# Performance work log

Hardware: AMD Instinct MI355X
Metric: run time of the kernel (lower is better)

Reference implementation:

```python
import jax, jax.numpy as jnp
import numpy as np

D = 1024
H = 16
HD = D // H  # 64
FF = 4 * D
EPS = 1e-5


def _xavier(key, shape):
    fan_in, fan_out = shape[1], shape[0]
    limit = float(np.sqrt(6.0 / (fan_in + fan_out)))
    return jax.random.uniform(key, shape, jnp.float32, -limit, limit)


def setup_inputs() -> dict:
    key = jax.random.key(0)
    ks = jax.random.split(key, 8)
    x = jax.random.normal(ks[0], (2, 2048, D), jnp.float32)
    return {
        "x": x,
        "w_qkv": _xavier(ks[1], (3 * D, D)),
        "b_qkv": jnp.zeros((3 * D,), jnp.float32),
        "w_out": _xavier(ks[2], (D, D)),
        "b_out": jnp.zeros((D,), jnp.float32),
        "w1": _xavier(ks[3], (FF, D)),
        "b1": jnp.zeros((FF,), jnp.float32),
        "w2": _xavier(ks[4], (D, FF)),
        "b2": jnp.zeros((D,), jnp.float32),
        "ln1_g": jnp.ones((D,), jnp.float32),
        "ln1_b": jnp.zeros((D,), jnp.float32),
        "ln2_g": jnp.ones((D,), jnp.float32),
        "ln2_b": jnp.zeros((D,), jnp.float32),
    }


def _layernorm(x, g, b):
    mu = jnp.mean(x, -1, keepdims=True)
    var = jnp.mean(jnp.square(x - mu), -1, keepdims=True)
    return (x - mu) * jax.lax.rsqrt(var + EPS) * g + b


def reference(x, w_qkv, b_qkv, w_out, b_out, w1, b1, w2, b2,
              ln1_g, ln1_b, ln2_g, ln2_b):
    B, S, _ = x.shape
    # pre-LN attention branch
    h = _layernorm(x, ln1_g, ln1_b)
    qkv = h @ w_qkv.T + b_qkv                      # [B,S,3D]
    qkv = qkv.reshape(B, S, H, 3 * HD).transpose(0, 2, 1, 3)  # [B,H,S,3hd]
    q, k, v = jnp.split(qkv, 3, axis=-1)
    scores = jnp.einsum('bhqd,bhkd->bhqk', q, k) / np.sqrt(HD)
    attn = jax.nn.softmax(scores, axis=-1)
    ctx = jnp.einsum('bhqk,bhkd->bhqd', attn, v)   # [B,H,S,hd]
    ctx = ctx.transpose(0, 2, 1, 3).reshape(B, S, D)
    x = x + (ctx @ w_out.T + b_out)
    # pre-LN MLP branch
    h = _layernorm(x, ln2_g, ln2_b)
    h = jax.nn.relu(h @ w1.T + b1)
    x = x + (h @ w2.T + b2)
    return x
```

## Files before the change

### kernel.cpp

```cpp
#include <hip/hip_runtime.h>
#include <hip/hip_bf16.h>

typedef __attribute__((ext_vector_type(8))) short bf16x8;
typedef __attribute__((ext_vector_type(4))) float f32x4;
typedef __attribute__((ext_vector_type(16))) float f32x16;
typedef __attribute__((ext_vector_type(4))) unsigned short u16x4;
typedef __attribute__((ext_vector_type(4))) unsigned int u32x4;
typedef unsigned short u16;

__device__ __forceinline__ u16 f2bf(float f) {
  unsigned u = __builtin_bit_cast(unsigned, f);
  u += 0x7fffu + ((u >> 16) & 1u);
  return (u16)(u >> 16);
}
__device__ __forceinline__ float bf2f(u16 u) {
  unsigned v = ((unsigned)u) << 16;
  return __builtin_bit_cast(float, v);
}
__device__ __forceinline__ unsigned cvt_pk_bf16(float lo, float hi) {
  unsigned r;
  asm("v_cvt_pk_bf16_f32 %0, %1, %2" : "=v"(r) : "v"(lo), "v"(hi));
  return r;
}
__device__ __forceinline__ float exp2_fast(float x) {
  float r;
  asm("v_exp_f32 %0, %1" : "=v"(r) : "v"(x));
  return r;
}

__device__ __forceinline__ void gl_lds16(const void* g, void* l) {
  __builtin_amdgcn_global_load_lds((const __attribute__((address_space(1))) void*)g,
                                   (__attribute__((address_space(3))) void*)l,
                                   16, 0, 0);
}

__device__ __forceinline__ void bar() {
  asm volatile("" ::: "memory");
  __builtin_amdgcn_s_barrier();
  asm volatile("" ::: "memory");
}

__global__ __launch_bounds__(256) void cvt_all(const float* __restrict__ a,
                                               const float* __restrict__ b,
                                               const float* __restrict__ c,
                                               const float* __restrict__ d,
                                               u16* __restrict__ oa,
                                               u16* __restrict__ ob,
                                               u16* __restrict__ oc,
                                               u16* __restrict__ od) {
  int i = blockIdx.x * 256 + threadIdx.x;
  const int stride = gridDim.x * 256;
  for (; i < 3145728; i += stride) {
    const float* src;
    u16* dst;
    int j;
    if (i < 786432) { src = a; dst = oa; j = i; }
    else if (i < 1048576) { src = b; dst = ob; j = i - 786432; }
    else if (i < 2097152) { src = c; dst = oc; j = i - 1048576; }
    else { src = d; dst = od; j = i - 2097152; }
    float4 v = ((const float4*)src)[j];
    u16x4 o;
    o.x = f2bf(v.x); o.y = f2bf(v.y); o.z = f2bf(v.z); o.w = f2bf(v.w);
    ((u16x4*)dst)[j] = o;
  }
}

__global__ __launch_bounds__(256) void ln_k(const float* __restrict__ x,
                                            const float* __restrict__ g,
                                            const float* __restrict__ b,
                                            u16* __restrict__ out) {
  const int row = blockIdx.x;
  const int t = threadIdx.x;
  const int lane = t & 63, w = t >> 6;
  const float4 v = ((const float4*)(x + (size_t)row * 1024))[t];
  float s = v.x + v.y + v.z + v.w;
  float q = v.x * v.x + v.y * v.y + v.z * v.z + v.w * v.w;
#pragma unroll
  for (int off = 32; off; off >>= 1) {
    s += __shfl_down(s, off);
    q += __shfl_down(q, off);
  }
  __shared__ float red[8];
  if (lane == 0) { red[w] = s; red[4 + w] = q; }
  __syncthreads();
  s = red[0] + red[1] + red[2] + red[3];
  q = red[4] + red[5] + red[6] + red[7];
  const float mu = s * (1.f / 1024.f);
  const float var = q * (1.f / 1024.f) - mu * mu;
  const float rs = rsqrtf(var + 1e-5f);
  const float4 gv = ((const float4*)g)[t];
  const float4 bv = ((const float4*)b)[t];
  u16x4 o;
  o.x = f2bf((v.x - mu) * rs * gv.x + bv.x);
  o.y = f2bf((v.y - mu) * rs * gv.y + bv.y);
  o.z = f2bf((v.z - mu) * rs * gv.z + bv.z);
  o.w = f2bf((v.w - mu) * rs * gv.w + bv.w);
  ((u16x4*)(out + (size_t)row * 1024))[t] = o;
}

template <int BM, int BN, int BK, int TH, int WN, int MR, int NR, int EPI>
__global__ __launch_bounds__(TH, 2) void gemm_rot(const u16* __restrict__ A,
                                                  const u16* __restrict__ B,
                                                  const float* __restrict__ bias,
                                                  const float* __restrict__ res,
                                                  void* __restrict__ outp,
                                                  const int N, const int K) {
  constexpr int GPR = BK / 8;
  constexpr int KS = BK / 32;
  constexpr int AELEMS = BM * BK;
  constexpr int BELEMS = BN * BK;
  constexpr int NC = (BM + BN) * GPR / TH;
  static_assert((BM * GPR) % TH == 0 && ((BM + BN) * GPR) % TH == 0, "");
  __shared__ u16 lds[3][AELEMS + BELEMS];
  const int t = threadIdx.x;
  const int lane = t & 63, w = t >> 6;
  const int wm = w / WN, wn = w % WN;
  const int l15 = lane & 15, lhi = lane >> 4;
  const int nbx = gridDim.x;
  const int nwg = nbx * gridDim.y;
  const int orig = blockIdx.y * nbx + blockIdx.x;
  const int cpx = nwg >> 3;
  const int lid = (orig & 7) * cpx + (orig >> 3);
  const long bm = (long)(lid / nbx) * BM, bn = (long)(lid % nbx) * BN;
  const u16* Ab = A + bm * K;
  const u16* Bb = B + bn * K;
  const int nk = K / BK;

#define STAGE(kt_, bufi)                                                      \
  do {                                                                        \
    const long kk_ = (long)(kt_) * BK;                                        \
    _Pragma("unroll")                                                         \
    for (int j = 0; j < NC; ++j) {                                            \
      const int sj = j * TH + t;                                              \
      const u16* src_;                                                        \
      if ((j + 1) * TH <= BM * GPR) {                                         \
        const int row_ = sj / GPR, grp_ = sj % GPR;                           \
        const int g_ = (BK == 32) ? (grp_ ^ ((row_ >> 1) & 3))                \
                                  : (grp_ ^ (row_ & 7));                      \
        src_ = Ab + (size_t)row_ * K + kk_ + g_ * 8;                          \
      } else {                                                                \
        const int sb_ = sj - BM * GPR;                                        \
        const int row_ = sb_ / GPR, grp_ = sb_ % GPR;                         \
        const int g_ = (BK == 32) ? (grp_ ^ ((row_ >> 1) & 3))                \
                                  : (grp_ ^ (row_ & 7));                      \
        src_ = Bb + (size_t)row_ * K + kk_ + g_ * 8;                          \
      }                                                                       \
      gl_lds16(src_, &lds[bufi][(size_t)(j * TH + w * 64) * 8]);              \
    }                                                                         \
  } while (0)

  f32x4 acc[MR][NR] = {};
  STAGE(0, 0);
  STAGE(1, 1);
  STAGE(2, 2);
  for (int i = 0; i < nk; ++i) {
    if (i + 2 < nk) {
      if constexpr (NC == 3)      asm volatile("s_waitcnt vmcnt(6)" ::: "memory");
      else if constexpr (NC == 4) asm volatile("s_waitcnt vmcnt(8)" ::: "memory");
      else                        asm volatile("s_waitcnt vmcnt(12)" ::: "memory");
    } else if (i + 1 < nk) {
      if constexpr (NC == 3)      asm volatile("s_waitcnt vmcnt(3)" ::: "memory");
      else if constexpr (NC == 4) asm volatile("s_waitcnt vmcnt(4)" ::: "memory");
      else                        asm volatile("s_waitcnt vmcnt(6)" ::: "memory");
    } else {
      asm volatile("s_waitcnt vmcnt(0)" ::: "memory");
    }
    bar();
    const u16* bufA = lds[i % 3];
    const u16* bufB = bufA + AELEMS;
    bf16x8 av[MR][KS], bv[NR][KS];
#pragma unroll
    for (int ii = 0; ii < MR; ++ii) {
      const int R = wm * (MR * 16) + ii * 16 + l15;
#pragma unroll
      for (int ks = 0; ks < KS; ++ks) {
        const int pos = (BK == 32) ? (lhi ^ ((R >> 1) & 3))
                                   : ((ks * 4 + lhi) ^ (R & 7));
        av[ii][ks] = *(const bf16x8*)&bufA[R * BK + (pos << 3)];
      }
    }
#pragma unroll
    for (int jj = 0; jj < NR; ++jj) {
      const int R = wn * (NR * 16) + jj * 16 + l15;
#pragma unroll
      for (int ks = 0; ks < KS; ++ks) {
        const int pos = (BK == 32) ? (lhi ^ ((R >> 1) & 3))
                                   : ((ks * 4 + lhi) ^ (R & 7));
        bv[jj][ks] = *(const bf16x8*)&bufB[R * BK + (pos << 3)];
      }
    }
    __builtin_amdgcn_s_setprio(1);
#pragma unroll
    for (int ii = 0; ii < MR; ++ii)
#pragma unroll
      for (int jj = 0; jj < NR; ++jj)
#pragma unroll
        for (int ks = 0; ks < KS; ++ks)
          acc[ii][jj] = __builtin_amdgcn_mfma_f32_16x16x32_bf16(av[ii][ks], bv[jj][ks],
                                                                acc[ii][jj], 0, 0, 0);
    __builtin_amdgcn_s_setprio(0);
    bar();
    if (i + 3 < nk) STAGE(i + 3, i % 3);
  }
#undef STAGE
#pragma unroll
  for (int jj = 0; jj < NR; ++jj) {
    const long col = bn + wn * (NR * 16) + jj * 16 + l15;
    const float bj = bias[col];
#pragma unroll
    for (int ii = 0; ii < MR; ++ii) {
      const long row0 = bm + wm * (MR * 16) + ii * 16 + lhi * 4;
#pragma unroll
      for (int r = 0; r < 4; ++r) {
        const float v = acc[ii][jj][r] + bj;
        const long idx = (row0 + r) * N + col;
        if constexpr (EPI == 0) {
          ((u16*)outp)[idx] = f2bf(v);
        } else if constexpr (EPI == 1) {
          ((float*)outp)[idx] = v + res[idx];
        } else {
          ((u16*)outp)[idx] = f2bf(v > 0.f ? v : 0.f);
        }
      }
    }
  }
}

__global__ __launch_bounds__(256) void vtrans(const u16* __restrict__ qkv,
                                              u16* __restrict__ vt) {
  const int t = threadIdx.x;
  const int bh = blockIdx.y, b = bh >> 4, h = bh & 15;
  const int kvb = blockIdx.x * 64;
  __shared__ u16 tile[64][72];
  const u16* src = qkv + ((size_t)(b * 2048 + kvb)) * 3072 + h * 192 + 128;
#pragma unroll
  for (int rr = 0; rr < 2; ++rr) {
    const int e = rr * 2048 + t * 8;
    const int kv = e >> 6, d = e & 63;
    *(bf16x8*)&tile[kv][d] = *(const bf16x8*)(src + (size_t)kv * 3072 + d);
  }
  __syncthreads();
#pragma unroll
  for (int rr = 0; rr < 2; ++rr) {
    const int e = rr * 2048 + t * 8;
    const int d = e >> 6, kv = e & 63;
    bf16x8 o;
#pragma unroll
    for (int j = 0; j < 8; ++j) o[j] = (short)tile[kv + j][d];
    *(bf16x8*)(vt + ((size_t)bh * 64 + d) * 2048 + kvb + kv) = o;
  }
}

__global__ __launch_bounds__(256, 4) void attn_k(const u16* __restrict__ qkv,
                                                 const u16* __restrict__ vt,
                                                 u16* __restrict__ part0,
                                                 u16* __restrict__ part1,
                                                 float* __restrict__ lbuf) {
  __shared__ u16 kt[2][4096];
  __shared__ u16 vtl[2][4096];
  const int t = threadIdx.x;
  const int lane = t & 63, w = t >> 6;
  const int l31 = lane & 31, hl = lane >> 5;
  const int l7 = l31 & 7;
  const int bh = blockIdx.y, b = bh >> 4, h = bh & 15;
  const int qb = blockIdx.x * 128 + w * 32;
  const int sidx = blockIdx.z;
  const int kvbeg = sidx * 1024, kvend = kvbeg + 1024;

  const float qscale = 0.125f * 1.44269504f;
  const u16* qp = qkv + ((size_t)(b * 2048 + qb + l31)) * 3072 + h * 192;
  bf16x8 qf[4];
#pragma unroll
  for (int ds = 0; ds < 4; ++ds) {
    bf16x8 v = *(const bf16x8*)(qp + 16 * ds + 8 * hl);
#pragma unroll
    for (int j = 0; j < 8; ++j) v[j] = (short)f2bf(bf2f((u16)v[j]) * qscale);
    qf[ds] = v;
  }

  const int srow = t >> 3, sgc = t & 7;
  const int sswz = (sgc ^ (srow & 7)) * 8;
  const u16* kg0 = qkv + ((size_t)(b * 2048 + srow)) * 3072 + h * 192 + 64 + sswz;
  const u16* vg0 = vt + (size_t)bh * 64 * 2048 + (size_t)srow * 2048 + sswz;

  f32x16 o0 = {}, o1 = {};
  float lsum = 0.f;

#define STAGE(bufi, kv0i)                                              \
  do {                                                                 \
    const u16* ks_ = kg0 + (size_t)(kv0i) * 3072;                      \
    const u16* vs_ = vg0 + (kv0i);                                     \
    gl_lds16(ks_, &kt[bufi][w * 512]);                                 \
    gl_lds16(ks_ + (size_t)32 * 3072, &kt[bufi][2048 + w * 512]);      \
    gl_lds16(vs_, &vtl[bufi][w * 512]);                                \
    gl_lds16(vs_ + (size_t)32 * 2048, &vtl[bufi][2048 + w * 512]);     \
  } while (0)

#define PACK(dst, SA, tl)                                                 \
  do {                                                                    \
    unsigned A0 = cvt_pk_bf16(SA[8 * tl + 0], SA[8 * tl + 1]);            \
    unsigned A1 = cvt_pk_bf16(SA[8 * tl + 2], SA[8 * tl + 3]);            \
    unsigned B0 = cvt_pk_bf16(SA[8 * tl + 4], SA[8 * tl + 5]);            \
    unsigned B1 = cvt_pk_bf16(SA[8 * tl + 6], SA[8 * tl + 7]);            \
    asm volatile("v_permlane32_swap_b32 %0, %1" : "+v"(A0), "+v"(B0));    \
    asm volatile("v_permlane32_swap_b32 %0, %1" : "+v"(A1), "+v"(B1));    \
    u32x4 pv_ = {A0, A1, B0, B1};                                         \
    dst = __builtin_bit_cast(bf16x8, pv_);                                \
  } while (0)

  int buf = 0;
  STAGE(0, kvbeg);
  for (int kv0 = kvbeg; kv0 < kvend; kv0 += 64) {
    if (kv0 + 64 < kvend) {
      STAGE(buf ^ 1, kv0 + 64);
      asm volatile("s_waitcnt vmcnt(4)" ::: "memory");
    } else {
      asm volatile("s_waitcnt vmcnt(0)" ::: "memory");
    }
    bar();
    f32x16 sa0 = {}, sa1 = {};
    __builtin_amdgcn_s_setprio(1);
#pragma unroll
    for (int ds = 0; ds < 4; ++ds) {
      const bf16x8 kf0 = *(const bf16x8*)&kt[buf][l31 * 64 + (((2 * ds + hl) ^ l7) << 3)];
      const bf16x8 kf1 = *(const bf16x8*)&kt[buf][(32 + l31) * 64 + (((2 * ds + hl) ^ l7) << 3)];
      sa0 = __builtin_amdgcn_mfma_f32_32x32x16_bf16(kf0, qf[ds], sa0, 0, 0, 0);
      sa1 = __builtin_amdgcn_mfma_f32_32x32x16_bf16(kf1, qf[ds], sa1, 0, 0, 0);
    }
    __builtin_amdgcn_s_setprio(0);
#pragma unroll
    for (int i = 0; i < 16; ++i) sa0[i] = exp2_fast(sa0[i]);
#pragma unroll
    for (int i = 0; i < 16; ++i) sa1[i] = exp2_fast(sa1[i]);
    const f32x16 ps = sa0 + sa1;
    float s8[8];
#pragma unroll
    for (int i = 0; i < 8; ++i) s8[i] = ps[i] + ps[i + 8];
    const float q0s = (s8[0] + s8[1]) + (s8[2] + s8[3]);
    const float q1s = (s8[4] + s8[5]) + (s8[6] + s8[7]);
    float rsum = q0s + q1s;
    rsum += __shfl_xor(rsum, 32);
    lsum += rsum;
    bf16x8 pf0, pf1, pf2, pf3;
    PACK(pf0, sa0, 0);
    PACK(pf1, sa0, 1);
    PACK(pf2, sa1, 0);
    PACK(pf3, sa1, 1);
    __builtin_amdgcn_s_setprio(1);
#pragma unroll
    for (int t4i = 0; t4i < 4; ++t4i) {
      const bf16x8 vf0 = *(const bf16x8*)&vtl[buf][l31 * 64 + (((2 * t4i + hl) ^ l7) << 3)];
      const bf16x8 vf1 = *(const bf16x8*)&vtl[buf][(32 + l31) * 64 + (((2 * t4i + hl) ^ l7) << 3)];
      const bf16x8 pf = (t4i == 0) ? pf0 : (t4i == 1) ? pf1 : (t4i == 2) ? pf2 : pf3;
      o0 = __builtin_amdgcn_mfma_f32_32x32x16_bf16(vf0, pf, o0, 0, 0, 0);
      o1 = __builtin_amdgcn_mfma_f32_32x32x16_bf16(vf1, pf, o1, 0, 0, 0);
    }
    __builtin_amdgcn_s_setprio(0);
    bar();
    buf ^= 1;
  }
#undef STAGE
#undef PACK
  if (lane < 32) {
    lbuf[(size_t)(sidx * 32 + bh) * 2048 + qb + l31] = lsum;
  }
  u16* obase = (sidx == 0) ? part0 : part1;
  u16* ow = ((u16*)kt) + w * 2048;
#pragma unroll
  for (int g2 = 0; g2 < 4; ++g2) {
    uint2 v0, v1;
    v0.x = cvt_pk_bf16(o0[4 * g2 + 0], o0[4 * g2 + 1]);
    v0.y = cvt_pk_bf16(o0[4 * g2 + 2], o0[4 * g2 + 3]);
    v1.x = cvt_pk_bf16(o1[4 * g2 + 0], o1[4 * g2 + 1]);
    v1.y = cvt_pk_bf16(o1[4 * g2 + 2], o1[4 * g2 + 3]);
    *(uint2*)&ow[l31 * 64 + ((g2 ^ l7) << 3) + hl * 4] = v0;
    *(uint2*)&ow[l31 * 64 + (((4 + g2) ^ l7) << 3) + hl * 4] = v1;
  }
#pragma unroll
  for (int p = 0; p < 4; ++p) {
    const int q = 8 * p + (lane >> 3);
    const int gpos = lane & 7;
    const bf16x8 val = *(const bf16x8*)&ow[q * 64 + (gpos << 3)];
    const int gd = gpos ^ (q & 7);
    *(bf16x8*)(obase + ((size_t)(b * 2048 + qb + q)) * 1024 + h * 64 + gd * 8) = val;
  }
}

__global__ __launch_bounds__(256) void attn_merge(const u16* __restrict__ p1,
                                                  const float* __restrict__ lbuf,
                                                  u16* __restrict__ ctx) {
  const int c = blockIdx.x * 256 + threadIdx.x;
  const int row = c >> 7;
  const int b = row >> 11, q = row & 2047;
  const int h = (c >> 3) & 15;
  const int bh = b * 16 + h;
  const float l1 = lbuf[(size_t)bh * 2048 + q];
  const float l2 = lbuf[(size_t)(32 + bh) * 2048 + q];
  const float inv = 1.f / (l1 + l2);
  const bf16x8 v0 = ((const bf16x8*)ctx)[c];
  const bf16x8 v1 = ((const bf16x8*)p1)[c];
  float r[8];
#pragma unroll
  for (int j = 0; j < 8; ++j)
    r[j] = (bf2f((u16)v0[j]) + bf2f((u16)v1[j])) * inv;
  u32x4 ov = {cvt_pk_bf16(r[0], r[1]), cvt_pk_bf16(r[2], r[3]),
              cvt_pk_bf16(r[4], r[5]), cvt_pk_bf16(r[6], r[7])};
  ((u32x4*)ctx)[c] = ov;
}

extern "C" void kernel_launch(void* const* d_in, const int* in_sizes, int n_in,
                              void* d_out, int out_size, void* d_ws, size_t ws_size,
                              hipStream_t stream) {
  const float* x     = (const float*)d_in[0];
  const float* w_qkv = (const float*)d_in[1];
  const float* b_qkv = (const float*)d_in[2];
  const float* w_out = (const float*)d_in[3];
  const float* b_out = (const float*)d_in[4];
  const float* w1    = (const float*)d_in[5];
  const float* b1    = (const float*)d_in[6];
  const float* w2    = (const float*)d_in[7];
  const float* b2    = (const float*)d_in[8];
  const float* ln1g  = (const float*)d_in[9];
  const float* ln1b  = (const float*)d_in[10];
  const float* ln2g  = (const float*)d_in[11];
  const float* ln2b  = (const float*)d_in[12];
  float* out = (float*)d_out;

  u16* wqkv_b = (u16*)d_ws;
  u16* wout_b = wqkv_b + (size_t)3072 * 1024;
  u16* w1_b   = wout_b + (size_t)1024 * 1024;
  u16* w2_b   = w1_b + (size_t)4096 * 1024;
  u16* r1     = w2_b + (size_t)1024 * 4096;
  u16* r2     = r1 + (size_t)4096 * 1024;
  u16* qkvb   = r2;
  u16* vtb    = r2 + (size_t)4096 * 3072;
  float* x2   = (float*)(r2 + (size_t)4096 * 4096);
  u16* part1  = (u16*)x2;
  float* lbuf = (float*)(part1 + (size_t)4096 * 1024);

  cvt_all<<<2048, 256, 0, stream>>>(w_qkv, w_out, w1, w2,
                                    wqkv_b, wout_b, w1_b, w2_b);

  ln_k<<<4096, 256, 0, stream>>>(x, ln1g, ln1b, r1);
  gemm_rot<128, 256, 32, 512, 4, 4, 4, 0><<<dim3(12, 32), 512, 0, stream>>>(
      r1, wqkv_b, b_qkv, nullptr, qkvb, 3072, 1024);
  vtrans<<<dim3(32, 32), 256, 0, stream>>>(qkvb, vtb);
  attn_k<<<dim3(16, 32, 2), 256, 0, stream>>>(qkvb, vtb, r1, part1, lbuf);
  attn_merge<<<2048, 256, 0, stream>>>(part1, lbuf, r1);
  gemm_rot<64, 128, 64, 256, 2, 2, 4, 1><<<dim3(8, 64), 256, 0, stream>>>(
      r1, wout_b, b_out, x, x2, 1024, 1024);
  ln_k<<<4096, 256, 0, stream>>>(x2, ln2g, ln2b, r1);
  gemm_rot<128, 256, 32, 512, 4, 4, 4, 2><<<dim3(16, 32), 512, 0, stream>>>(
      r1, w1_b, b1, nullptr, r2, 4096, 1024);
  gemm_rot<64, 128, 64, 256, 2, 2, 4, 1><<<dim3(8, 64), 256, 0, stream>>>(
      r2, w2_b, b2, x2, out, 1024, 4096);
}
```

Before: 211.8 us.

## Fuse weight conversion into first layernorm and compute softmax row sums via MFMA

Merges the fp32-to-bf16 weight conversion kernel with the first layernorm kernel into one launch, with blocks split by index, removing one launch and letting the two memory-bound phases overlap. In attention, the per-row exp sum is no longer computed with VALU adds and a lane shuffle. It is taken from an extra MFMA against a ones vector that accumulates the bf16-rounded probabilities. This trades VALU reduction work for one extra matrix op per V step, and the row sum now uses bf16-rounded values, which matches the numerator.

```diff
diff --git a/kernel.cpp b/kernel.cpp
--- a/kernel.cpp
+++ b/kernel.cpp
@@ -40,28 +40,62 @@
   asm volatile("" ::: "memory");
 }
 
-__global__ __launch_bounds__(256) void cvt_all(const float* __restrict__ a,
-                                               const float* __restrict__ b,
-                                               const float* __restrict__ c,
-                                               const float* __restrict__ d,
-                                               u16* __restrict__ oa,
-                                               u16* __restrict__ ob,
-                                               u16* __restrict__ oc,
-                                               u16* __restrict__ od) {
-  int i = blockIdx.x * 256 + threadIdx.x;
-  const int stride = gridDim.x * 256;
-  for (; i < 3145728; i += stride) {
-    const float* src;
-    u16* dst;
-    int j;
-    if (i < 786432) { src = a; dst = oa; j = i; }
-    else if (i < 1048576) { src = b; dst = ob; j = i - 786432; }
-    else if (i < 2097152) { src = c; dst = oc; j = i - 1048576; }
-    else { src = d; dst = od; j = i - 2097152; }
-    float4 v = ((const float4*)src)[j];
+__global__ __launch_bounds__(256) void ln_cvt(const float* __restrict__ x,
+                                              const float* __restrict__ g,
+                                              const float* __restrict__ b,
+                                              u16* __restrict__ out,
+                                              const float* __restrict__ wa,
+                                              const float* __restrict__ wb,
+                                              const float* __restrict__ wc,
+                                              const float* __restrict__ wd,
+                                              u16* __restrict__ oa,
+                                              u16* __restrict__ ob,
+                                              u16* __restrict__ oc,
+                                              u16* __restrict__ od) {
+  __shared__ float red[8];
+  const int t = threadIdx.x;
+  if (blockIdx.x < 4096) {
+    const int row = blockIdx.x;
+    const int lane = t & 63, w = t >> 6;
+    const float4 v = ((const float4*)(x + (size_t)row * 1024))[t];
+    float s = v.x + v.y + v.z + v.w;
+    float q = v.x * v.x + v.y * v.y + v.z * v.z + v.w * v.w;
+#pragma unroll
+    for (int off = 32; off; off >>= 1) {
+      s += __shfl_down(s, off);
+      q += __shfl_down(q, off);
+    }
+    if (lane == 0) { red[w] = s; red[4 + w] = q; }
+    __syncthreads();
+    s = red[0] + red[1] + red[2] + red[3];
+    q = red[4] + red[5] + red[6] + red[7];
+    const float mu = s * (1.f / 1024.f);
+    const float var = q * (1.f / 1024.f) - mu * mu;
+    const float rs = rsqrtf(var + 1e-5f);
+    const float4 gv = ((const float4*)g)[t];
+    const float4 bv = ((const float4*)b)[t];
     u16x4 o;
-    o.x = f2bf(v.x); o.y = f2bf(v.y); o.z = f2bf(v.z); o.w = f2bf(v.w);
-    ((u16x4*)dst)[j] = o;
+    o.x = f2bf((v.x - mu) * rs * gv.x + bv.x);
+    o.y = f2bf((v.y - mu) * rs * gv.y + bv.y);
+    o.z = f2bf((v.z - mu) * rs * gv.z + bv.z);
+    o.w = f2bf((v.w - mu) * rs * gv.w + bv.w);
+    ((u16x4*)(out + (size_t)row * 1024))[t] = o;
+  } else {
+    int i = (blockIdx.x - 4096) * 256 + t;
+    const int stride = 2048 * 256;
+    for (; i < 3145728; i += stride) {
+      const float* src;
+      u16* dst;
+      int j;
+      if (i < 786432) { src = wa; dst = oa; j = i; }
+      else if (i < 1048576) { src = wb; dst = ob; j = i - 786432; }
+      else if (i < 2097152) { src = wc; dst = oc; j = i - 1048576; }
+      else { src = wd; dst = od; j = i - 2097152; }
+      float4 v = ((const float4*)src)[j];
+      u16x4 o;
+      o.x = f2bf(v.x); o.y = f2bf(v.y); o.z = f2bf(v.z); o.w = f2bf(v.w);
+      ((u16x4*)dst)[j] = o;
+    }
   }
 }
 
@@ -277,14 +311,16 @@
     for (int j = 0; j < 8; ++j) v[j] = (short)f2bf(bf2f((u16)v[j]) * qscale);
     qf[ds] = v;
   }
+  bf16x8 ones;
+#pragma unroll
+  for (int j = 0; j < 8; ++j) ones[j] = (short)0x3F80;
 
   const int srow = t >> 3, sgc = t & 7;
   const int sswz = (sgc ^ (srow & 7)) * 8;
   const u16* kg0 = qkv + ((size_t)(b * 2048 + srow)) * 3072 + h * 192 + 64 + sswz;
   const u16* vg0 = vt + (size_t)bh * 64 * 2048 + (size_t)srow * 2048 + sswz;
 
-  f32x16 o0 = {}, o1 = {};
-  float lsum = 0.f;
+  f32x16 o0 = {}, o1 = {}, ol = {};
 
 #define STAGE(bufi, kv0i)                                              \
   do {                                                                 \
@@ -332,15 +368,6 @@
     for (int i = 0; i < 16; ++i) sa0[i] = exp2_fast(sa0[i]);
 #pragma unroll
     for (int i = 0; i < 16; ++i) sa1[i] = exp2_fast(sa1[i]);
-    const f32x16 ps = sa0 + sa1;
-    float s8[8];
-#pragma unroll
-    for (int i = 0; i < 8; ++i) s8[i] = ps[i] + ps[i + 8];
-    const float q0s = (s8[0] + s8[1]) + (s8[2] + s8[3]);
-    const float q1s = (s8[4] + s8[5]) + (s8[6] + s8[7]);
-    float rsum = q0s + q1s;
-    rsum += __shfl_xor(rsum, 32);
-    lsum += rsum;
     bf16x8 pf0, pf1, pf2, pf3;
     PACK(pf0, sa0, 0);
     PACK(pf1, sa0, 1);
@@ -354,6 +381,7 @@
       const bf16x8 pf = (t4i == 0) ? pf0 : (t4i == 1) ? pf1 : (t4i == 2) ? pf2 : pf3;
       o0 = __builtin_amdgcn_mfma_f32_32x32x16_bf16(vf0, pf, o0, 0, 0, 0);
       o1 = __builtin_amdgcn_mfma_f32_32x32x16_bf16(vf1, pf, o1, 0, 0, 0);
+      ol = __builtin_amdgcn_mfma_f32_32x32x16_bf16(ones, pf, ol, 0, 0, 0);
     }
     __builtin_amdgcn_s_setprio(0);
     bar();
@@ -362,7 +390,7 @@
 #undef STAGE
 #undef PACK
   if (lane < 32) {
-    lbuf[(size_t)(sidx * 32 + bh) * 2048 + qb + l31] = lsum;
+    lbuf[(size_t)(sidx * 32 + bh) * 2048 + qb + l31] = ol[0];
   }
   u16* obase = (sidx == 0) ? part0 : part1;
   u16* ow = ((u16*)kt) + w * 2048;
@@ -438,10 +466,10 @@
   u16* part1  = (u16*)x2;
   float* lbuf = (float*)(part1 + (size_t)4096 * 1024);
 
-  cvt_all<<<2048, 256, 0, stream>>>(w_qkv, w_out, w1, w2,
-                                    wqkv_b, wout_b, w1_b, w2_b);
-
-  ln_k<<<4096, 256, 0, stream>>>(x, ln1g, ln1b, r1);
+  ln_cvt<<<6144, 256, 0, stream>>>(x, ln1g, ln1b, r1,
+                                   w_qkv, w_out, w1, w2,
+                                   wqkv_b, wout_b, w1_b, w2_b);
+
   gemm_rot<128, 256, 32, 512, 4, 4, 4, 0><<<dim3(12, 32), 512, 0, stream>>>(
       r1, wqkv_b, b_qkv, nullptr, qkvb, 3072, 1024);
   vtrans<<<dim3(32, 32), 256, 0, stream>>>(qkvb, vtb);
```

New measurement: 212.1 us. No clear change (+0.2%).
